# Performance work log

Hardware: AMD Instinct MI355X
Metric: run time of the kernel (lower is better)

## Reference

```python
import jax, jax.numpy as jnp
import numpy as np

B, S, D = 1, 2048, 4096
H, KVH, HD = 32, 8, 128
GROUPS = H // KVH  # 4
SCALE = HD ** -0.5
NEG = jnp.finfo(jnp.float32).min


def rotate_half(x):
    x1 = x[..., : x.shape[-1] // 2]
    x2 = x[..., x.shape[-1] // 2:]
    return jnp.concatenate((-x2, x1), axis=-1)


def setup_inputs() -> dict:
    key = jax.random.key(0)
    ks = jax.random.split(key, 8)
    return {
        "hidden_states": jax.random.normal(ks[0], (B, S, D), dtype=jnp.float32),
        "cos": jax.random.uniform(ks[1], (B, S, HD), dtype=jnp.float32),
        "sin": jax.random.uniform(ks[2], (B, S, HD), dtype=jnp.float32),
        "attention_mask": jnp.ones((B, S), dtype=bool),
        "wq": jax.random.normal(ks[3], (D, H * HD), dtype=jnp.float32) * 0.02,
        "wk": jax.random.normal(ks[4], (D, KVH * HD), dtype=jnp.float32) * 0.02,
        "wv": jax.random.normal(ks[5], (D, KVH * HD), dtype=jnp.float32) * 0.02,
        "wo": jax.random.normal(ks[6], (H * HD, D), dtype=jnp.float32) * 0.02,
    }


def reference(hidden_states, cos, sin, attention_mask, wq, wk, wv, wo):
    b, s, _ = hidden_states.shape
    # projections -> (B,S,heads,head_dim)
    q = (hidden_states @ wq).reshape(b, s, H, HD)
    k = (hidden_states @ wk).reshape(b, s, KVH, HD)
    v = (hidden_states @ wv).reshape(b, s, KVH, HD)
    # RoPE (cos/sin unsqueezed at head axis)
    c = cos[:, :, None, :]
    si = sin[:, :, None, :]
    q = q * c + rotate_half(q) * si
    k = k * c + rotate_half(k) * si
    # GQA: repeat kv heads (cache_index=0, max_len==S -> cache write is identity)
    k = jnp.repeat(k, GROUPS, axis=2)
    v = jnp.repeat(v, GROUPS, axis=2)
    # mask: causal AND padding; bias 0 / -inf
    causal = jnp.tril(jnp.ones((s, s), dtype=bool))[None, None]  # (1,1,S,S)
    mask = causal & attention_mask[:, None, None, :]  # (B,1,S,S)
    bias = jnp.where(mask, 0.0, NEG).astype(hidden_states.dtype)
    # scores (B,H,S,S)
    scores = jnp.einsum("bqhd,bkhd->bhqk", q, k) * SCALE + bias
    attn = jax.nn.softmax(scores, axis=-1)
    out = jnp.einsum("bhqk,bkhd->bqhd", attn, v).reshape(b, s, H * HD)
    return out @ wo
```

## Files before the change

kernel.cpp:

```cpp
#include <hip/hip_runtime.h>
#include <hip/hip_bf16.h>

#define SEQ   2048
#define DM    4096
#define NH    32
#define NKVH  8
#define HD    128
#define NQKV  6144
#define KOFF  4096
#define VOFF  5120
#define QLD   5120
#define SCALE 0.08838834764831845f

typedef __attribute__((ext_vector_type(4))) float f32x4;
typedef __attribute__((ext_vector_type(8))) short short8;

__device__ __forceinline__ unsigned short f2bf(float f) {
  union { float f; unsigned int u; } v; v.f = f;
  unsigned int r = v.u + 0x7FFF + ((v.u >> 16) & 1);
  return (unsigned short)(r >> 16);
}
__device__ __forceinline__ float bf2f(unsigned short b) {
  union { unsigned int u; float f; } v; v.u = ((unsigned int)b) << 16;
  return v.f;
}

__device__ __forceinline__ void gld16(const unsigned short* g, unsigned short* l) {
  __builtin_amdgcn_global_load_lds(
      (const __attribute__((address_space(1))) unsigned int*)g,
      (__attribute__((address_space(3))) unsigned int*)l, 16, 0, 0);
}

__global__ __launch_bounds__(256) void prep(const float* __restrict__ hs,
                                            const float* __restrict__ wq,
                                            const float* __restrict__ wk,
                                            const float* __restrict__ wv,
                                            const float* __restrict__ wo,
                                            unsigned short* __restrict__ hsb,
                                            unsigned short* __restrict__ wqkvT,
                                            unsigned short* __restrict__ woT) {
  __shared__ unsigned short t2[64][72];
  const int bxg = blockIdx.x;
  const int tid = threadIdx.x;
  if (bxg < 8192) {
    size_t i = ((size_t)bxg * 256 + tid) * 4;
    float4 v = *(const float4*)(hs + i);
    ushort4 o;
    o.x = f2bf(v.x); o.y = f2bf(v.y); o.z = f2bf(v.z); o.w = f2bf(v.w);
    *(ushort4*)(hsb + i) = o;
    return;
  }
  const int b  = bxg - 8192;
  const int bx = b % 160;
  const int k0 = (b / 160) * 64;
  const float* W; unsigned short* out; int N, n0, row_off;
  if (bx < 64)      { W = wq; out = wqkvT; N = 4096; n0 = bx * 64;        row_off = 0;    }
  else if (bx < 80) { W = wk; out = wqkvT; N = 1024; n0 = (bx - 64) * 64; row_off = 4096; }
  else if (bx < 96) { W = wv; out = wqkvT; N = 1024; n0 = (bx - 80) * 64; row_off = 5120; }
  else              { W = wo; out = woT;   N = 4096; n0 = (bx - 96) * 64; row_off = 0;    }

  const int n  = tid & 63;
  const int q  = tid >> 6;
#pragma unroll
  for (int i = 0; i < 4; ++i) {
    const int kq = (i * 4 + q) * 4;
    float f0 = W[(size_t)(k0 + kq + 0) * N + n0 + n];
    float f1 = W[(size_t)(k0 + kq + 1) * N + n0 + n];
    float f2 = W[(size_t)(k0 + kq + 2) * N + n0 + n];
    float f3 = W[(size_t)(k0 + kq + 3) * N + n0 + n];
    ushort4 u; u.x = f2bf(f0); u.y = f2bf(f1); u.z = f2bf(f2); u.w = f2bf(f3);
    *(ushort4*)&t2[n][kq] = u;
  }
  __syncthreads();

  const int sn = tid >> 3;
  const int c8 = (tid & 7) * 8;
#pragma unroll
  for (int i = 0; i < 2; ++i) {
    const int nn = sn + i * 32;
    short8 v = *(const short8*)&t2[nn][c8];
    *(short8*)&out[(size_t)(row_off + n0 + nn) * DM + k0 + c8] = v;
  }
}

__global__ __launch_bounds__(256) void gemm_bt(const unsigned short* __restrict__ A,
                                               const unsigned short* __restrict__ Bt,
                                               void* __restrict__ C,
                                               unsigned short* __restrict__ vt,
                                               int M, int N, int K, int ldc, int c_fp32) {
  __shared__ unsigned short As[2][128 * 32];
  __shared__ unsigned short Bs[2][128 * 32];
  const int tid  = threadIdx.x;
  const int m0   = blockIdx.y * 128;
  const int n0   = blockIdx.x * 128;
  const int w    = tid >> 6;
  const int lane = tid & 63;
  const int l16  = lane & 15;
  const int quad = lane >> 4;
  const int wr   = (w >> 1) * 64;
  const int wc   = (w & 1) * 64;

  f32x4 acc[4][4];
#pragma unroll
  for (int i = 0; i < 4; ++i)
#pragma unroll
    for (int j = 0; j < 4; ++j) acc[i][j] = (f32x4){0.f, 0.f, 0.f, 0.f};

  const int sr  = lane >> 2;
  const int pb  = lane & 3;
  const int sws = (sr & 3) ^ ((sr >> 2) & 3);
  const int kb  = ((pb ^ sws) << 3);
  const unsigned short* ga0 = A  + (size_t)(m0 + w * 16 + sr) * K + kb;
  const unsigned short* ga1 = A  + (size_t)(m0 + 64 + w * 16 + sr) * K + kb;
  const unsigned short* gb0 = Bt + (size_t)(n0 + w * 16 + sr) * K + kb;
  const unsigned short* gb1 = Bt + (size_t)(n0 + 64 + w * 16 + sr) * K + kb;
  const int lofs0 = (w * 16) * 32;
  const int lofs1 = (64 + w * 16) * 32;

  const int swf  = (l16 & 3) ^ ((l16 >> 2) & 3);
  const int fcol = ((quad ^ swf) << 3);

  gld16(ga0, &As[0][lofs0]);
  gld16(ga1, &As[0][lofs1]);
  gld16(gb0, &Bs[0][lofs0]);
  gld16(gb1, &Bs[0][lofs1]);

  int p = 0;
  for (int k0 = 0; k0 < K; k0 += 32) {
    __syncthreads();
    if (k0 + 32 < K) {
      gld16(ga0 + k0 + 32, &As[p ^ 1][lofs0]);
      gld16(ga1 + k0 + 32, &As[p ^ 1][lofs1]);
      gld16(gb0 + k0 + 32, &Bs[p ^ 1][lofs0]);
      gld16(gb1 + k0 + 32, &Bs[p ^ 1][lofs1]);
    }
    short8 af[4], bfr[4];
#pragma unroll
    for (int mt = 0; mt < 4; ++mt)
      af[mt] = *(const short8*)&As[p][(wr + mt * 16 + l16) * 32 + fcol];
#pragma unroll
    for (int nt = 0; nt < 4; ++nt)
      bfr[nt] = *(const short8*)&Bs[p][(wc + nt * 16 + l16) * 32 + fcol];
#pragma unroll
    for (int mt = 0; mt < 4; ++mt)
#pragma unroll
      for (int nt = 0; nt < 4; ++nt)
        acc[mt][nt] = __builtin_amdgcn_mfma_f32_16x16x32_bf16(af[mt], bfr[nt], acc[mt][nt], 0, 0, 0);
    p ^= 1;
  }

  if (vt && n0 >= VOFF) {
#pragma unroll
    for (int mt = 0; mt < 4; ++mt)
#pragma unroll
      for (int nt = 0; nt < 4; ++nt) {
        int col  = (n0 - VOFF) + wc + nt * 16 + l16;
        int row0 = m0 + wr + mt * 16 + quad * 4;
        ushort4 ov;
        ov.x = f2bf(acc[mt][nt][0]); ov.y = f2bf(acc[mt][nt][1]);
        ov.z = f2bf(acc[mt][nt][2]); ov.w = f2bf(acc[mt][nt][3]);
        *(ushort4*)&vt[(size_t)col * SEQ + row0] = ov;
      }
  } else if (c_fp32) {
    float* Cf = (float*)C;
#pragma unroll
    for (int mt = 0; mt < 4; ++mt)
#pragma unroll
      for (int nt = 0; nt < 4; ++nt) {
        int col = n0 + wc + nt * 16 + l16;
#pragma unroll
        for (int r = 0; r < 4; ++r)
          Cf[(size_t)(m0 + wr + mt * 16 + quad * 4 + r) * ldc + col] = acc[mt][nt][r];
      }
  } else {
    unsigned short* Cb = (unsigned short*)C;
#pragma unroll
    for (int mt = 0; mt < 4; ++mt)
#pragma unroll
      for (int nt = 0; nt < 4; ++nt) {
        int col = n0 + wc + nt * 16 + l16;
#pragma unroll
        for (int r = 0; r < 4; ++r)
          Cb[(size_t)(m0 + wr + mt * 16 + quad * 4 + r) * ldc + col] = f2bf(acc[mt][nt][r]);
      }
  }
}

__global__ __launch_bounds__(256) void rope_k(unsigned short* __restrict__ QKV,
                                              const float* __restrict__ cosb,
                                              const float* __restrict__ sinb) {
  int idx = blockIdx.x * 256 + threadIdx.x;
  int i  = idx & 63;
  int hk = (idx >> 6) & 7;
  int s  = idx >> 9;
  size_t base = (size_t)s * QLD + KOFF + (size_t)hk * 128;
  float q1 = bf2f(QKV[base + i]);
  float q2 = bf2f(QKV[base + i + 64]);
  float c1 = cosb[s * 128 + i],      s1 = sinb[s * 128 + i];
  float c2 = cosb[s * 128 + i + 64], s2 = sinb[s * 128 + i + 64];
  QKV[base + i]      = f2bf(q1 * c1 - q2 * s1);
  QKV[base + i + 64] = f2bf(q2 * c2 + q1 * s2);
}

__global__ __launch_bounds__(256) void flash_attn(const unsigned short* __restrict__ QKV,
                                                  const unsigned short* __restrict__ Vt_g,
                                                  const float* __restrict__ cosb,
                                                  const float* __restrict__ sinb,
                                                  unsigned short* __restrict__ AO) {
  __shared__ unsigned short Ks[64 * 136];
  __shared__ unsigned short Vs[128 * 72];
  __shared__ unsigned short Ps[4][32 * 68];

  const int h   = blockIdx.x;
  const int qt  = (int)gridDim.y - 1 - (int)blockIdx.y;
  const int kvh = h >> 2;
  const int tid  = threadIdx.x;
  const int w    = tid >> 6;
  const int lane = tid & 63;
  const int l16  = lane & 15;
  const int quad = lane >> 4;
  const int q0   = qt * 128;
  const int qrow_w = q0 + w * 32;

  short8 qf[2][4];
#pragma unroll
  for (int ntq = 0; ntq < 2; ++ntq) {
    const int s_row = qrow_w + ntq * 16 + l16;
    const unsigned short* qp = QKV + (size_t)s_row * QLD + h * HD + quad * 8;
#pragma unroll
    for (int ks = 0; ks < 4; ++ks) qf[ntq][ks] = *(const short8*)(qp + ks * 32);
    const float* cb = cosb + (size_t)s_row * 128 + quad * 8;
    const float* sb = sinb + (size_t)s_row * 128 + quad * 8;
#pragma unroll
    for (int ks = 0; ks < 2; ++ks) {
#pragma unroll
      for (int e = 0; e < 8; ++e) {
        int d = ks * 32 + e;
        float f1 = bf2f((unsigned short)qf[ntq][ks][e]);
        float f2 = bf2f((unsigned short)qf[ntq][ks + 2][e]);
        float c1 = cb[d],      s1v = sb[d];
        float c2 = cb[d + 64], s2v = sb[d + 64];
        qf[ntq][ks][e]     = (short)f2bf(f1 * c1 - f2 * s1v);
        qf[ntq][ks + 2][e] = (short)f2bf(f2 * c2 + f1 * s2v);
      }
    }
  }

  f32x4 o[8][2];
#pragma unroll
  for (int i = 0; i < 8; ++i) { o[i][0] = (f32x4){0,0,0,0}; o[i][1] = (f32x4){0,0,0,0}; }
  float m_i[2] = {-3.0e38f, -3.0e38f}, l_i[2] = {0.f, 0.f};

  const int kr = tid >> 2, kcol0 = (tid & 3) * 32;
  const int vr = tid >> 1, vcol0 = (tid & 1) * 32;
  const unsigned short* kbase = QKV + KOFF + (size_t)kvh * HD + kcol0;
  const unsigned short* vbase = Vt_g + ((size_t)kvh * HD + vr) * SEQ + vcol0;

  const int nch = qt * 2 + 2;

  short8 kv[4], vv[4];
#pragma unroll
  for (int u = 0; u < 4; ++u) kv[u] = *(const short8*)(kbase + (size_t)kr * QLD + u * 8);
#pragma unroll
  for (int u = 0; u < 4; ++u) vv[u] = *(const short8*)(vbase + u * 8);

  for (int c = 0; c < nch; ++c) {
    const int kc = c * 64;
    __builtin_amdgcn_s_barrier();
#pragma unroll
    for (int u = 0; u < 4; ++u) *(short8*)&Ks[kr * 136 + kcol0 + u * 8] = kv[u];
#pragma unroll
    for (int u = 0; u < 4; ++u) *(short8*)&Vs[vr * 72 + vcol0 + u * 8] = vv[u];
    if (c + 1 < nch) {
      const int kn = kc + 64;
#pragma unroll
      for (int u = 0; u < 4; ++u) kv[u] = *(const short8*)(kbase + (size_t)(kn + kr) * QLD + u * 8);
#pragma unroll
      for (int u = 0; u < 4; ++u) vv[u] = *(const short8*)(vbase + kn + u * 8);
    }
    asm volatile("s_waitcnt lgkmcnt(0)" ::: "memory");
    __builtin_amdgcn_s_barrier();

    if (kc <= qrow_w + 31) {
      f32x4 st[4][2];
#pragma unroll
      for (int mt = 0; mt < 4; ++mt) { st[mt][0] = (f32x4){0,0,0,0}; st[mt][1] = (f32x4){0,0,0,0}; }
      __builtin_amdgcn_s_setprio(1);
#pragma unroll
      for (int ks = 0; ks < 4; ++ks)
#pragma unroll
        for (int mt = 0; mt < 4; ++mt) {
          short8 ak = *(const short8*)&Ks[(mt * 16 + l16) * 136 + ks * 32 + quad * 8];
          st[mt][0] = __builtin_amdgcn_mfma_f32_16x16x32_bf16(ak, qf[0][ks], st[mt][0], 0, 0, 0);
          st[mt][1] = __builtin_amdgcn_mfma_f32_16x16x32_bf16(ak, qf[1][ks], st[mt][1], 0, 0, 0);
        }
      __builtin_amdgcn_s_setprio(0);

      float sc[4][2][4];
      const bool fullch = (kc + 64 <= qrow_w);
      if (fullch) {
#pragma unroll
        for (int mt = 0; mt < 4; ++mt)
#pragma unroll
          for (int ntq = 0; ntq < 2; ++ntq)
#pragma unroll
            for (int r = 0; r < 4; ++r) sc[mt][ntq][r] = st[mt][ntq][r] * SCALE;
      } else {
#pragma unroll
        for (int mt = 0; mt < 4; ++mt)
#pragma unroll
          for (int ntq = 0; ntq < 2; ++ntq) {
            int qr = qrow_w + ntq * 16 + l16;
#pragma unroll
            for (int r = 0; r < 4; ++r) {
              int key = kc + mt * 16 + quad * 4 + r;
              float v = st[mt][ntq][r] * SCALE;
              sc[mt][ntq][r] = (key <= qr) ? v : -__builtin_inff();
            }
          }
      }
      float mx[2] = {-__builtin_inff(), -__builtin_inff()};
#pragma unroll
      for (int mt = 0; mt < 4; ++mt)
#pragma unroll
        for (int ntq = 0; ntq < 2; ++ntq)
#pragma unroll
          for (int r = 0; r < 4; ++r) mx[ntq] = fmaxf(mx[ntq], sc[mt][ntq][r]);
#pragma unroll
      for (int ntq = 0; ntq < 2; ++ntq) {
        mx[ntq] = fmaxf(mx[ntq], __shfl_xor(mx[ntq], 16, 64));
        mx[ntq] = fmaxf(mx[ntq], __shfl_xor(mx[ntq], 32, 64));
      }

      bool upd = (mx[0] > m_i[0] + 8.f) || (mx[1] > m_i[1] + 8.f);
      if (__any(upd ? 1 : 0)) {
        float al[2];
#pragma unroll
        for (int ntq = 0; ntq < 2; ++ntq) {
          float mn = fmaxf(m_i[ntq], mx[ntq]);
          al[ntq] = __expf(m_i[ntq] - mn);
          m_i[ntq] = mn;
          l_i[ntq] *= al[ntq];
        }
#pragma unroll
        for (int i = 0; i < 8; ++i) {
          o[i][0][0] *= al[0]; o[i][0][1] *= al[0]; o[i][0][2] *= al[0]; o[i][0][3] *= al[0];
          o[i][1][0] *= al[1]; o[i][1][1] *= al[1]; o[i][1][2] *= al[1]; o[i][1][3] *= al[1];
        }
      }

      float rs[2] = {0.f, 0.f};
      unsigned short* psw = &Ps[w][0];
#pragma unroll
      for (int mt = 0; mt < 4; ++mt)
#pragma unroll
        for (int ntq = 0; ntq < 2; ++ntq) {
          float p0 = __expf(sc[mt][ntq][0] - m_i[ntq]);
          float p1 = __expf(sc[mt][ntq][1] - m_i[ntq]);
          float p2 = __expf(sc[mt][ntq][2] - m_i[ntq]);
          float p3 = __expf(sc[mt][ntq][3] - m_i[ntq]);
          rs[ntq] += (p0 + p1) + (p2 + p3);
          ushort4 pk; pk.x = f2bf(p0); pk.y = f2bf(p1); pk.z = f2bf(p2); pk.w = f2bf(p3);
          *(ushort4*)&psw[(ntq * 16 + l16) * 68 + mt * 16 + quad * 4] = pk;
        }
#pragma unroll
      for (int ntq = 0; ntq < 2; ++ntq) {
        rs[ntq] += __shfl_xor(rs[ntq], 16, 64);
        rs[ntq] += __shfl_xor(rs[ntq], 32, 64);
        l_i[ntq] += rs[ntq];
      }

#pragma unroll
      for (int ks = 0; ks < 2; ++ks) {
        short8 bp[2];
#pragma unroll
        for (int ntq = 0; ntq < 2; ++ntq) {
          union { ushort4 h[2]; short8 v; } u;
          const unsigned short* pp = &psw[(ntq * 16 + l16) * 68 + ks * 32 + quad * 8];
          u.h[0] = *(const ushort4*)(pp);
          u.h[1] = *(const ushort4*)(pp + 4);
          bp[ntq] = u.v;
        }
        __builtin_amdgcn_s_setprio(1);
#pragma unroll
        for (int mt = 0; mt < 8; ++mt) {
          short8 av = *(const short8*)&Vs[(mt * 16 + l16) * 72 + ks * 32 + quad * 8];
          o[mt][0] = __builtin_amdgcn_mfma_f32_16x16x32_bf16(av, bp[0], o[mt][0], 0, 0, 0);
          o[mt][1] = __builtin_amdgcn_mfma_f32_16x16x32_bf16(av, bp[1], o[mt][1], 0, 0, 0);
        }
        __builtin_amdgcn_s_setprio(0);
      }
    }
  }

  float inv[2] = {1.0f / l_i[0], 1.0f / l_i[1]};
#pragma unroll
  for (int mt = 0; mt < 8; ++mt)
#pragma unroll
    for (int ntq = 0; ntq < 2; ++ntq) {
      int qr = qrow_w + ntq * 16 + l16;
      int col = h * HD + mt * 16 + quad * 4;
      ushort4 ov;
      ov.x = f2bf(o[mt][ntq][0] * inv[ntq]);
      ov.y = f2bf(o[mt][ntq][1] * inv[ntq]);
      ov.z = f2bf(o[mt][ntq][2] * inv[ntq]);
      ov.w = f2bf(o[mt][ntq][3] * inv[ntq]);
      *(ushort4*)&AO[(size_t)qr * DM + col] = ov;
    }
}

extern "C" void kernel_launch(void* const* d_in, const int* in_sizes, int n_in,
                              void* d_out, int out_size, void* d_ws, size_t ws_size,
                              hipStream_t stream) {
  const float* hs   = (const float*)d_in[0];
  const float* cosb = (const float*)d_in[1];
  const float* sinb = (const float*)d_in[2];
  const float* wq = (const float*)d_in[4];
  const float* wk = (const float*)d_in[5];
  const float* wv = (const float*)d_in[6];
  const float* wo = (const float*)d_in[7];
  float* out = (float*)d_out;

  char* ws = (char*)d_ws;
  unsigned short* hsb   = (unsigned short*)(ws);
  unsigned short* wqkvT = (unsigned short*)(ws + (16u << 20));
  unsigned short* woT   = (unsigned short*)(ws + (64u << 20));
  unsigned short* qkv   = (unsigned short*)(ws + (96u << 20));
  unsigned short* ao    = (unsigned short*)(ws + (116u << 20));
  unsigned short* Vt_g  = (unsigned short*)(ws + (132u << 20));

  prep<<<8192 + 160 * 64, 256, 0, stream>>>(hs, wq, wk, wv, wo, hsb, wqkvT, woT);
  gemm_bt<<<dim3(NQKV / 128, SEQ / 128), 256, 0, stream>>>(hsb, wqkvT, qkv, Vt_g, SEQ, NQKV, DM, QLD, 0);
  rope_k<<<4096, 256, 0, stream>>>(qkv, cosb, sinb);
  flash_attn<<<dim3(NH, SEQ / 128), 256, 0, stream>>>(qkv, Vt_g, cosb, sinb, ao);
  gemm_bt<<<dim3(DM / 128, SEQ / 128), 256, 0, stream>>>(ao, woT, out, nullptr, SEQ, DM, DM, DM, 1);
}
```

Before: 524.0 us.

## Triple-buffer GEMM LDS tiles with explicit vmcnt waits and raw barriers

The bf16 GEMM main loop moves from double-buffered to triple-buffered LDS staging, unrolled by three. Each stage uses `s_waitcnt vmcnt(4)` plus `s_barrier` instead of `__syncthreads`, so loads for the tile two steps ahead stay in flight during the MFMA work. The goal is to hide more global-load latency. In exchange, LDS per block grows by half, which may reduce occupancy, and the loop count is hardcoded for K=4096.

```diff
diff --git a/kernel.cpp b/kernel.cpp
--- a/kernel.cpp
+++ b/kernel.cpp
@@ -88,8 +88,12 @@
                                                void* __restrict__ C,
                                                unsigned short* __restrict__ vt,
                                                int M, int N, int K, int ldc, int c_fp32) {
-  __shared__ unsigned short As[2][128 * 32];
-  __shared__ unsigned short Bs[2][128 * 32];
+  __shared__ unsigned short As0[128 * 32];
+  __shared__ unsigned short As1[128 * 32];
+  __shared__ unsigned short As2[128 * 32];
+  __shared__ unsigned short Bs0[128 * 32];
+  __shared__ unsigned short Bs1[128 * 32];
+  __shared__ unsigned short Bs2[128 * 32];
   const int tid  = threadIdx.x;
   const int m0   = blockIdx.y * 128;
   const int n0   = blockIdx.x * 128;
@@ -120,34 +124,54 @@
   const int swf  = (l16 & 3) ^ ((l16 >> 2) & 3);
   const int fcol = ((quad ^ swf) << 3);
 
-  gld16(ga0, &As[0][lofs0]);
-  gld16(ga1, &As[0][lofs1]);
-  gld16(gb0, &Bs[0][lofs0]);
-  gld16(gb1, &Bs[0][lofs1]);
-
-  int p = 0;
-  for (int k0 = 0; k0 < K; k0 += 32) {
-    __syncthreads();
-    if (k0 + 32 < K) {
-      gld16(ga0 + k0 + 32, &As[p ^ 1][lofs0]);
-      gld16(ga1 + k0 + 32, &As[p ^ 1][lofs1]);
-      gld16(gb0 + k0 + 32, &Bs[p ^ 1][lofs0]);
-      gld16(gb1 + k0 + 32, &Bs[p ^ 1][lofs1]);
-    }
-    short8 af[4], bfr[4];
-#pragma unroll
-    for (int mt = 0; mt < 4; ++mt)
-      af[mt] = *(const short8*)&As[p][(wr + mt * 16 + l16) * 32 + fcol];
-#pragma unroll
-    for (int nt = 0; nt < 4; ++nt)
-      bfr[nt] = *(const short8*)&Bs[p][(wc + nt * 16 + l16) * 32 + fcol];
-#pragma unroll
-    for (int mt = 0; mt < 4; ++mt)
-#pragma unroll
-      for (int nt = 0; nt < 4; ++nt)
-        acc[mt][nt] = __builtin_amdgcn_mfma_f32_16x16x32_bf16(af[mt], bfr[nt], acc[mt][nt], 0, 0, 0);
-    p ^= 1;
-  }
+#define STG(AS, BS, ko)                                \
+  do {                                                 \
+    gld16(ga0 + (ko), &AS[lofs0]);                     \
+    gld16(ga1 + (ko), &AS[lofs1]);                     \
+    gld16(gb0 + (ko), &BS[lofs0]);                     \
+    gld16(gb1 + (ko), &BS[lofs1]);                     \
+  } while (0)
+
+#define CMP(AS, BS)                                                            \
+  do {                                                                         \
+    short8 af[4], bfr[4];                                                      \
+    _Pragma("unroll") for (int mt = 0; mt < 4; ++mt)                           \
+        af[mt] = *(const short8*)&AS[(wr + mt * 16 + l16) * 32 + fcol];        \
+    _Pragma("unroll") for (int nt = 0; nt < 4; ++nt)                           \
+        bfr[nt] = *(const short8*)&BS[(wc + nt * 16 + l16) * 32 + fcol];       \
+    _Pragma("unroll") for (int mt = 0; mt < 4; ++mt)                           \
+        _Pragma("unroll") for (int nt = 0; nt < 4; ++nt)                       \
+            acc[mt][nt] = __builtin_amdgcn_mfma_f32_16x16x32_bf16(             \
+                af[mt], bfr[nt], acc[mt][nt], 0, 0, 0);                        \
+  } while (0)
+
+  STG(As0, Bs0, 0);
+  STG(As1, Bs1, 32);
+
+  int k0 = 0;
+  for (int it = 0; it < 126; it += 3) {
+    asm volatile("s_waitcnt vmcnt(4)" ::: "memory");
+    __builtin_amdgcn_s_barrier();
+    STG(As2, Bs2, k0 + 64);
+    CMP(As0, Bs0);
+    asm volatile("s_waitcnt vmcnt(4)" ::: "memory");
+    __builtin_amdgcn_s_barrier();
+    STG(As0, Bs0, k0 + 96);
+    CMP(As1, Bs1);
+    asm volatile("s_waitcnt vmcnt(4)" ::: "memory");
+    __builtin_amdgcn_s_barrier();
+    STG(As1, Bs1, k0 + 128);
+    CMP(As2, Bs2);
+    k0 += 96;
+  }
+  asm volatile("s_waitcnt vmcnt(4)" ::: "memory");
+  __builtin_amdgcn_s_barrier();
+  CMP(As0, Bs0);
+  asm volatile("s_waitcnt vmcnt(0)" ::: "memory");
+  __builtin_amdgcn_s_barrier();
+  CMP(As1, Bs1);
+#undef STG
+#undef CMP
 
   if (vt && n0 >= VOFF) {
 #pragma unroll
```

Result: no change. 531.3 us (+1.4%).
